# Kernel optimization log

Hardware: AMD Instinct MI355X
Metric: run time of the kernel (lower is better)

The kernel has to match this reference:

```python
import jax, jax.numpy as jnp
import numpy as np

Z_DIM = 128
OUT_DIM = 64
CHANNELS = 3
N_LINEARS = 16
BATCH = 1024
OUT_FEATS = CHANNELS * OUT_DIM * OUT_DIM * N_LINEARS  # 196608


def setup_inputs() -> dict:
    key = jax.random.key(0)
    k_z, k_c, k_w, k_b = jax.random.split(key, 4)
    z = jax.random.normal(k_z, (BATCH, Z_DIM), dtype=jnp.float32)
    # torch.randint(0, n_linears - 1, ...) -> values in [0, 14]
    c = jax.random.randint(k_c, (BATCH,), 0, N_LINEARS - 1, dtype=jnp.int64)
    W = jax.random.normal(k_w, (OUT_FEATS, Z_DIM), dtype=jnp.float32) * 0.02
    b = jax.random.normal(k_b, (OUT_FEATS,), dtype=jnp.float32) * 0.02
    return {"z": z, "c": c, "W": W, "b": b}


def reference(z, c, W, b):
    # Dense linear producing n_linears 'expert' outputs per sample
    out = jnp.einsum('bz,oz->bo', z, W) + b               # [B, O*N]
    out = out.reshape(-1, N_LINEARS, CHANNELS, OUT_DIM, OUT_DIM)
    # Per-sample gather of the selected expert slice
    return out[jnp.arange(out.shape[0]), c]               # [B, C, H, W]
```

## Files before the change

### kernel.cpp

```cpp
#include <hip/hip_runtime.h>


#define Z_DIM 128
#define OPE   12288
#define NEXP  16
#define NT    256
#define MTILE 16
#define NCOLS 64
#define WPAD  136

typedef __attribute__((ext_vector_type(8))) short short8;
typedef __attribute__((ext_vector_type(4))) float f32x4;
typedef unsigned short u16;
typedef unsigned int   u32;

__device__ __forceinline__ void split_f32(float f, u16& h, u16& l) {
    union { float f; u32 u; } a, b, r;
    a.f = f;
    h = (u16)(a.u >> 16);
    b.u = ((u32)h) << 16;
    r.f = f - b.f;
    l = (u16)((r.u + 0x8000u) >> 16);
}

__global__ __launch_bounds__(NT, 2)
void expert_mfma(const float* __restrict__ z,
                 const int* __restrict__ c,
                 const float* __restrict__ W,
                 const float* __restrict__ bias,
                 float* __restrict__ out,
                 int B) {
    __shared__ int lst[1024];
    __shared__ int cnt_sh;
    __shared__ __align__(16) u16 Whi[NCOLS][WPAD];
    __shared__ __align__(16) u16 Wlo[NCOLS][WPAD];
    __shared__ __align__(16) u16 Zhi[MTILE][WPAD];
    __shared__ __align__(16) u16 Zlo[MTILE][WPAD];

    const int tid = threadIdx.x;
    const int e   = blockIdx.y;
    const int n0  = blockIdx.x * NCOLS;

    if (tid == 0) cnt_sh = 0;
    __syncthreads();
    for (int i = tid; i < B; i += NT)
        if (c[i] == e) lst[atomicAdd(&cnt_sh, 1)] = i;
    __syncthreads();
    const int cnt = cnt_sh;
    if (cnt == 0) return;

    #pragma unroll
    for (int it = 0; it < 8; ++it) {
        const int chunk = it * NT + tid;
        const int row = chunk >> 5;
        const int kc  = chunk & 31;
        const float4 v = *(const float4*)(W + ((size_t)e * OPE + n0 + row) * Z_DIM + kc * 4);
        u16 h0,h1,h2,h3,l0,l1,l2,l3;
        split_f32(v.x,h0,l0); split_f32(v.y,h1,l1);
        split_f32(v.z,h2,l2); split_f32(v.w,h3,l3);
        uint2 hv, lv;
        hv.x = (u32)h0 | ((u32)h1 << 16); hv.y = (u32)h2 | ((u32)h3 << 16);
        lv.x = (u32)l0 | ((u32)l1 << 16); lv.y = (u32)l2 | ((u32)l3 << 16);
        *(uint2*)&Whi[row][kc * 4] = hv;
        *(uint2*)&Wlo[row][kc * 4] = lv;
    }

    const int lane = tid & 63;
    const int wv   = tid >> 6;
    const int fr   = lane & 15;
    const int kg   = lane >> 4;

    const int   col = n0 + wv * 16 + fr;
    const float bv  = bias[(size_t)e * OPE + col];

    const int zr = tid >> 4;
    const int zk = (tid & 15) * 8;

    for (int m0 = 0; m0 < cnt; m0 += MTILE) {
        __syncthreads();

        {
            const int r = m0 + zr;
            float4 v0 = {0.f,0.f,0.f,0.f}, v1 = {0.f,0.f,0.f,0.f};
            if (r < cnt) {
                const float* zp = z + (size_t)lst[r] * Z_DIM + zk;
                v0 = *(const float4*)zp;
                v1 = *(const float4*)(zp + 4);
            }
            u16 h[8], l[8];
            split_f32(v0.x,h[0],l[0]); split_f32(v0.y,h[1],l[1]);
            split_f32(v0.z,h[2],l[2]); split_f32(v0.w,h[3],l[3]);
            split_f32(v1.x,h[4],l[4]); split_f32(v1.y,h[5],l[5]);
            split_f32(v1.z,h[6],l[6]); split_f32(v1.w,h[7],l[7]);
            uint4 hv, lv;
            hv.x=(u32)h[0]|((u32)h[1]<<16); hv.y=(u32)h[2]|((u32)h[3]<<16);
            hv.z=(u32)h[4]|((u32)h[5]<<16); hv.w=(u32)h[6]|((u32)h[7]<<16);
            lv.x=(u32)l[0]|((u32)l[1]<<16); lv.y=(u32)l[2]|((u32)l[3]<<16);
            lv.z=(u32)l[4]|((u32)l[5]<<16); lv.w=(u32)l[6]|((u32)l[7]<<16);
            *(uint4*)&Zhi[zr][zk] = hv;
            *(uint4*)&Zlo[zr][zk] = lv;
        }
        __syncthreads();

        f32x4 acc = {0.f, 0.f, 0.f, 0.f};
        #pragma unroll
        for (int kk = 0; kk < 4; ++kk) {
            const int ko = kk * 32 + kg * 8;
            const short8 ah = *(const short8*)&Zhi[fr][ko];
            const short8 al = *(const short8*)&Zlo[fr][ko];
            const short8 bh = *(const short8*)&Whi[wv * 16 + fr][ko];
            const short8 bl = *(const short8*)&Wlo[wv * 16 + fr][ko];
            acc = __builtin_amdgcn_mfma_f32_16x16x32_bf16(ah, bh, acc, 0, 0, 0);
            acc = __builtin_amdgcn_mfma_f32_16x16x32_bf16(ah, bl, acc, 0, 0, 0);
            acc = __builtin_amdgcn_mfma_f32_16x16x32_bf16(al, bh, acc, 0, 0, 0);
        }

        #pragma unroll
        for (int j = 0; j < 4; ++j) {
            const int r = m0 + kg * 4 + j;
            if (r < cnt)
                out[(size_t)lst[r] * OPE + col] = acc[j] + bv;
        }
    }
}

extern "C" void kernel_launch(void* const* d_in, const int* in_sizes, int n_in,
                              void* d_out, int out_size, void* d_ws, size_t ws_size,
                              hipStream_t stream) {
    const float* z = (const float*)d_in[0];
    const int*   c = (const int*)d_in[1];
    const float* W = (const float*)d_in[2];
    const float* b = (const float*)d_in[3];
    float* out = (float*)d_out;
    const int B = in_sizes[0] / Z_DIM;

    dim3 grid(OPE / NCOLS, NEXP);
    expert_mfma<<<grid, NT, 0, stream>>>(z, c, W, b, out, B);
}
```

Measured before the change: 190.3 us.

## Keep W fragments in registers and stage larger Z chunks in shared memory

Each lane now loads and splits its W row slice directly into registers as MFMA B operands, which removes the W shared-memory tiles and their LDS traffic. Z rows are staged in chunks of 64 instead of 16, so there are fewer barriers per expert, and the index list is stored as 16-bit values to shrink LDS. The smaller LDS footprint allows raising launch bounds to 4 blocks per CU for more occupancy, at the cost of register pressure from holding 8 short8 fragments per lane.

```diff
diff --git a/kernel.cpp b/kernel.cpp
--- a/kernel.cpp
+++ b/kernel.cpp
@@ -1,13 +1,13 @@
 #include <hip/hip_runtime.h>
 
 
-#define Z_DIM 128
-#define OPE   12288
-#define NEXP  16
-#define NT    256
-#define MTILE 16
-#define NCOLS 64
-#define WPAD  136
+#define Z_DIM  128
+#define OPE    12288
+#define NEXP   16
+#define NT     256
+#define NCOLS  64
+#define MCHUNK 64
+#define WPAD   136
 
 typedef __attribute__((ext_vector_type(8))) short short8;
 typedef __attribute__((ext_vector_type(4))) float f32x4;
@@ -23,19 +23,17 @@
     l = (u16)((r.u + 0x8000u) >> 16);
 }
 
-__global__ __launch_bounds__(NT, 2)
+__global__ __launch_bounds__(NT, 4)
 void expert_mfma(const float* __restrict__ z,
                  const int* __restrict__ c,
                  const float* __restrict__ W,
                  const float* __restrict__ bias,
                  float* __restrict__ out,
                  int B) {
-    __shared__ int lst[1024];
+    __shared__ u16 lst[1024];
     __shared__ int cnt_sh;
-    __shared__ __align__(16) u16 Whi[NCOLS][WPAD];
-    __shared__ __align__(16) u16 Wlo[NCOLS][WPAD];
-    __shared__ __align__(16) u16 Zhi[MTILE][WPAD];
-    __shared__ __align__(16) u16 Zlo[MTILE][WPAD];
+    __shared__ __align__(16) u16 Zhi[MCHUNK][WPAD];
+    __shared__ __align__(16) u16 Zlo[MCHUNK][WPAD];
 
     const int tid = threadIdx.x;
     const int e   = blockIdx.y;
@@ -44,26 +42,10 @@
     if (tid == 0) cnt_sh = 0;
     __syncthreads();
     for (int i = tid; i < B; i += NT)
-        if (c[i] == e) lst[atomicAdd(&cnt_sh, 1)] = i;
+        if (c[i] == e) lst[atomicAdd(&cnt_sh, 1)] = (u16)i;
     __syncthreads();
     const int cnt = cnt_sh;
     if (cnt == 0) return;
-
-    #pragma unroll
-    for (int it = 0; it < 8; ++it) {
-        const int chunk = it * NT + tid;
-        const int row = chunk >> 5;
-        const int kc  = chunk & 31;
-        const float4 v = *(const float4*)(W + ((size_t)e * OPE + n0 + row) * Z_DIM + kc * 4);
-        u16 h0,h1,h2,h3,l0,l1,l2,l3;
-        split_f32(v.x,h0,l0); split_f32(v.y,h1,l1);
-        split_f32(v.z,h2,l2); split_f32(v.w,h3,l3);
-        uint2 hv, lv;
-        hv.x = (u32)h0 | ((u32)h1 << 16); hv.y = (u32)h2 | ((u32)h3 << 16);
-        lv.x = (u32)l0 | ((u32)l1 << 16); lv.y = (u32)l2 | ((u32)l3 << 16);
-        *(uint2*)&Whi[row][kc * 4] = hv;
-        *(uint2*)&Wlo[row][kc * 4] = lv;
-    }
 
     const int lane = tid & 63;
     const int wv   = tid >> 6;
@@ -73,53 +55,79 @@
     const int   col = n0 + wv * 16 + fr;
     const float bv  = bias[(size_t)e * OPE + col];
 
-    const int zr = tid >> 4;
-    const int zk = (tid & 15) * 8;
-
-    for (int m0 = 0; m0 < cnt; m0 += MTILE) {
-        __syncthreads();
-
-        {
-            const int r = m0 + zr;
-            float4 v0 = {0.f,0.f,0.f,0.f}, v1 = {0.f,0.f,0.f,0.f};
-            if (r < cnt) {
-                const float* zp = z + (size_t)lst[r] * Z_DIM + zk;
-                v0 = *(const float4*)zp;
-                v1 = *(const float4*)(zp + 4);
-            }
+    short8 bh[4], bl[4];
+    {
+        const float* wrow = W + ((size_t)e * OPE + col) * Z_DIM;
+        #pragma unroll
+        for (int kk = 0; kk < 4; ++kk) {
+            const float* p = wrow + kk * 32 + kg * 8;
+            const float4 v0 = *(const float4*)p;
+            const float4 v1 = *(const float4*)(p + 4);
             u16 h[8], l[8];
             split_f32(v0.x,h[0],l[0]); split_f32(v0.y,h[1],l[1]);
             split_f32(v0.z,h[2],l[2]); split_f32(v0.w,h[3],l[3]);
             split_f32(v1.x,h[4],l[4]); split_f32(v1.y,h[5],l[5]);
             split_f32(v1.z,h[6],l[6]); split_f32(v1.w,h[7],l[7]);
-            uint4 hv, lv;
-            hv.x=(u32)h[0]|((u32)h[1]<<16); hv.y=(u32)h[2]|((u32)h[3]<<16);
-            hv.z=(u32)h[4]|((u32)h[5]<<16); hv.w=(u32)h[6]|((u32)h[7]<<16);
-            lv.x=(u32)l[0]|((u32)l[1]<<16); lv.y=(u32)l[2]|((u32)l[3]<<16);
-            lv.z=(u32)l[4]|((u32)l[5]<<16); lv.w=(u32)l[6]|((u32)l[7]<<16);
-            *(uint4*)&Zhi[zr][zk] = hv;
-            *(uint4*)&Zlo[zr][zk] = lv;
+            short8 hh, ll;
+            hh[0]=(short)h[0]; hh[1]=(short)h[1]; hh[2]=(short)h[2]; hh[3]=(short)h[3];
+            hh[4]=(short)h[4]; hh[5]=(short)h[5]; hh[6]=(short)h[6]; hh[7]=(short)h[7];
+            ll[0]=(short)l[0]; ll[1]=(short)l[1]; ll[2]=(short)l[2]; ll[3]=(short)l[3];
+            ll[4]=(short)l[4]; ll[5]=(short)l[5]; ll[6]=(short)l[6]; ll[7]=(short)l[7];
+            bh[kk] = hh; bl[kk] = ll;
+        }
+    }
+
+    const int zr = tid >> 2;
+    const int zq = (tid & 3) * 32;
+
+    for (int m0 = 0; m0 < cnt; m0 += MCHUNK) {
+        __syncthreads();
+
+        {
+            const int  r     = m0 + zr;
+            const bool valid = r < cnt;
+            const float* zp  = z + (valid ? (size_t)lst[r] * Z_DIM + zq : 0);
+            #pragma unroll
+            for (int q = 0; q < 4; ++q) {
+                float4 v0 = {0.f,0.f,0.f,0.f}, v1 = {0.f,0.f,0.f,0.f};
+                if (valid) {
+                    v0 = *(const float4*)(zp + q * 8);
+                    v1 = *(const float4*)(zp + q * 8 + 4);
+                }
+                u16 h[8], l[8];
+                split_f32(v0.x,h[0],l[0]); split_f32(v0.y,h[1],l[1]);
+                split_f32(v0.z,h[2],l[2]); split_f32(v0.w,h[3],l[3]);
+                split_f32(v1.x,h[4],l[4]); split_f32(v1.y,h[5],l[5]);
+                split_f32(v1.z,h[6],l[6]); split_f32(v1.w,h[7],l[7]);
+                uint4 hv, lv;
+                hv.x=(u32)h[0]|((u32)h[1]<<16); hv.y=(u32)h[2]|((u32)h[3]<<16);
+                hv.z=(u32)h[4]|((u32)h[5]<<16); hv.w=(u32)h[6]|((u32)h[7]<<16);
+                lv.x=(u32)l[0]|((u32)l[1]<<16); lv.y=(u32)l[2]|((u32)l[3]<<16);
+                lv.z=(u32)l[4]|((u32)l[5]<<16); lv.w=(u32)l[6]|((u32)l[7]<<16);
+                *(uint4*)&Zhi[zr][zq + q * 8] = hv;
+                *(uint4*)&Zlo[zr][zq + q * 8] = lv;
+            }
         }
         __syncthreads();
 
-        f32x4 acc = {0.f, 0.f, 0.f, 0.f};
-        #pragma unroll
-        for (int kk = 0; kk < 4; ++kk) {
-            const int ko = kk * 32 + kg * 8;
-            const short8 ah = *(const short8*)&Zhi[fr][ko];
-            const short8 al = *(const short8*)&Zlo[fr][ko];
-            const short8 bh = *(const short8*)&Whi[wv * 16 + fr][ko];
-            const short8 bl = *(const short8*)&Wlo[wv * 16 + fr][ko];
-            acc = __builtin_amdgcn_mfma_f32_16x16x32_bf16(ah, bh, acc, 0, 0, 0);
-            acc = __builtin_amdgcn_mfma_f32_16x16x32_bf16(ah, bl, acc, 0, 0, 0);
-            acc = __builtin_amdgcn_mfma_f32_16x16x32_bf16(al, bh, acc, 0, 0, 0);
-        }
-
-        #pragma unroll
-        for (int j = 0; j < 4; ++j) {
-            const int r = m0 + kg * 4 + j;
-            if (r < cnt)
-                out[(size_t)lst[r] * OPE + col] = acc[j] + bv;
+        const int mlim = min(cnt - m0, MCHUNK);
+        for (int ms = 0; ms < mlim; ms += 16) {
+            f32x4 acc = {0.f, 0.f, 0.f, 0.f};
+            #pragma unroll
+            for (int kk = 0; kk < 4; ++kk) {
+                const int ko = kk * 32 + kg * 8;
+                const short8 ah = *(const short8*)&Zhi[ms + fr][ko];
+                const short8 al = *(const short8*)&Zlo[ms + fr][ko];
+                acc = __builtin_amdgcn_mfma_f32_16x16x32_bf16(ah, bh[kk], acc, 0, 0, 0);
+                acc = __builtin_amdgcn_mfma_f32_16x16x32_bf16(ah, bl[kk], acc, 0, 0, 0);
+                acc = __builtin_amdgcn_mfma_f32_16x16x32_bf16(al, bh[kk], acc, 0, 0, 0);
+            }
+            #pragma unroll
+            for (int j = 0; j < 4; ++j) {
+                const int r = m0 + ms + kg * 4 + j;
+                if (r < cnt)
+                    out[(size_t)lst[r] * OPE + col] = acc[j] + bv;
+            }
         }
     }
 }
```

After: 181.1 us. 4.8% less time.
